# Kernel tuning notes

Hardware: AMD Instinct MI355X
Metric: run time of the kernel (lower is better)

## Reference

```python
import jax, jax.numpy as jnp
import numpy as np
from jax import lax

KS = 3      # generated depthwise kernel size
F = 9       # utils.FILTERS (channels)
P = 24      # utils.PSZ (patch size); conv stride 8 -> KS = P/8


def _extract_patches(x, p):
    # TF extract_patches with sizes=strides=p, VALID: (B,H,W,C) -> (B,nh,nw,p*p*C)
    B, H, W, C = x.shape
    nh, nw = H // p, W // p
    return (x.reshape(B, nh, p, nw, p, C)
             .transpose(0, 1, 3, 2, 4, 5)
             .reshape(B, nh, nw, p * p * C))


def setup_inputs() -> dict:
    key = jax.random.key(0)
    ks = jax.random.split(key, 6)
    B, H, Wd = 16, 384, 384
    return {
        "guidance": jax.random.normal(ks[0], (B, H, Wd, F), jnp.float32),
        "depth": jax.random.normal(ks[1], (B, H, Wd, F), jnp.float32),
        "conv_w": jax.random.normal(ks[2], (KS, KS, F, 9), jnp.float32) * 0.05,
        "conv_b": jax.random.normal(ks[3], (9,), jnp.float32) * 0.05,
        "dense_w": jax.random.normal(ks[4], (F, F * F), jnp.float32) * 0.05,
        "dense_b": jax.random.normal(ks[5], (F * F,), jnp.float32) * 0.05,
    }


def _forward(guidance, depth, conv_w, conv_b, dense_w, dense_b):
    B, H, W, _ = guidance.shape
    NP = (H // P) * (W // P)
    NB = NP * B
    # raw TF reshape (B,nh,nw,P*P*F) -> (NP,B,P,P,F), reproduced faithfully
    gp = _extract_patches(guidance, P).reshape(NP, B, P, P, F)
    dp = _extract_patches(depth, P).reshape(NP, B, P, P, F)

    # --- KGL: per-patch kernel generation (vectorized over NP*B) ---
    gflat = gp.reshape(NB, P, P, F)
    c = lax.conv_general_dilated(gflat, conv_w, (8, 8), 'SAME',
                                 dimension_numbers=('NHWC', 'HWIO', 'NHWC')) + conv_b
    W_G1 = c.reshape(NP, B, KS, KS, F, 1)
    n1 = jnp.sqrt(jnp.sum(W_G1 * W_G1, axis=(2, 3), keepdims=True))
    W_G1 = W_G1 / jnp.maximum(n1, 1.0)          # tf.clip_by_norm(.., 1, axes=[1,2])

    gap = gp.mean(axis=(2, 3))                   # (NP,B,F)
    d = gap @ dense_w + dense_b                  # (NP,B,F*F)
    W_G2 = d.reshape(NP, B, 1, 1, F, F)
    n2 = jnp.sqrt(jnp.sum(W_G2 * W_G2, axis=(2, 3, 4), keepdims=True))
    W_G2 = W_G2 / jnp.maximum(n2, 1.0)           # clip_by_norm axes=[1,2,3]

    # --- per-sample dynamic depthwise conv (vmap over NP*B) ---
    dw_rhs = W_G1.reshape(NB, KS, KS, F, 1).transpose(0, 1, 2, 4, 3)  # HWIO, groups=F
    dflat = dp.reshape(NB, P, P, F)

    def dwconv(img, f):
        return lax.conv_general_dilated(img[None], f, (1, 1), 'SAME',
                                        dimension_numbers=('NHWC', 'HWIO', 'NHWC'),
                                        feature_group_count=F)[0]

    dc = jax.vmap(dwconv)(dflat, dw_rhs)         # (NB,P,P,F)

    # --- per-sample dynamic 1x1 cross-channel conv == matmul ---
    cc = jnp.einsum('npqi,nio->npqo', dc, W_G2.reshape(NB, F, F))
    # raw TF reshape (NP,B,P,P,F) -> (B,H,W,F), reproduced faithfully
    return cc.reshape(B, H, W, F)


def reference(guidance, depth, conv_w, conv_b, dense_w, dense_b):
    return _forward(guidance, depth, conv_w, conv_b, dense_w, dense_b)
```

## Files before the change

kernel.cpp:

```cpp
#include <hip/hip_runtime.h>
#include <stdint.h>


__global__ __launch_bounds__(256) void kgl_kernel(
    const float* __restrict__ g,
    const float* __restrict__ cw,
    const float* __restrict__ cb,
    const float* __restrict__ dw,
    const float* __restrict__ db,
    float* __restrict__ ws)
{
    __shared__ __align__(16) float sg[5184];
    __shared__ float cwf[729];
    __shared__ float cbf[9];
    __shared__ float dwf[729];
    __shared__ float dbf[81];
    __shared__ float cols[216];
    __shared__ float gapm[9];
    __shared__ float cful[81];
    __shared__ float dld[81];

    const int m = blockIdx.x;
    const int t = threadIdx.x;
    const int b0 = m >> 8, pi = (m >> 4) & 15, pj = m & 15;
    const long rowbase = ((long)(b0 * 384 + pi * 24)) * 3456 + (long)pj * 216;

    for (int task = t; task < 1296; task += 256) {
        int r = task / 54, c = task - r * 54;
        const float4* p = reinterpret_cast<const float4*>(g + rowbase + (long)r * 3456);
        reinterpret_cast<float4*>(sg + r * 216)[c] = p[c];
    }
    for (int idx = t; idx < 729; idx += 256) cwf[idx] = cw[idx];
    for (int idx = t; idx < 729; idx += 256) dwf[idx] = dw[idx];
    if (t < 9) cbf[t] = cb[t];
    if (t >= 32 && t < 113) dbf[t - 32] = db[t - 32];
    if (t < 216 && (t % 12) >= 9) ws[(long)m * 216 + t] = 0.0f;
    __syncthreads();

    if (t < 216) {
        float s = 0.f;
        #pragma unroll
        for (int r = 0; r < 24; ++r) s += sg[r * 216 + t];
        cols[t] = s;
    }
    __syncthreads();

    if (t < 81) {
        int o = t % 9, uv = t / 9, v = uv % 3, u = uv / 3;
        float acc = cbf[o];
        #pragma unroll
        for (int du = 0; du < 3; ++du)
        #pragma unroll
        for (int dv = 0; dv < 3; ++dv) {
            const float* gp2 = &sg[(u * 8 + du) * 216 + (v * 8 + dv) * 9];
            const float* wp  = &cwf[(du * 3 + dv) * 81 + o];
            #pragma unroll
            for (int ci = 0; ci < 9; ++ci) acc += gp2[ci] * wp[ci * 9];
        }
        cful[t] = acc;
    }
    if (t >= 216 && t < 225) {
        int f = t - 216; float s = 0.f;
        #pragma unroll
        for (int c = 0; c < 24; ++c) s += cols[c * 9 + f];
        gapm[f] = s * (1.0f / 576.0f);
    }
    __syncthreads();

    if (t < 81) {
        float acc = dbf[t];
        #pragma unroll
        for (int k = 0; k < 9; ++k) acc += gapm[k] * dwf[k * 81 + t];
        dld[t] = acc;
    }
    if (t >= 96 && t < 105) {
        int f = t - 96; float s = 0.f;
        #pragma unroll
        for (int k = 0; k < 9; ++k) { float c = cful[k * 9 + f]; s += c * c; }
        float scale = (s > 1.0f) ? (1.0f / sqrtf(s)) : 1.0f;
        float* wout = ws + (long)m * 216;
        #pragma unroll
        for (int k = 0; k < 9; ++k) wout[k * 12 + f] = cful[k * 9 + f] * scale;
    }
    __syncthreads();

    if (t < 9) {
        float s = 0.f;
        #pragma unroll
        for (int i = 0; i < 9; ++i) { float d = dld[i * 9 + t]; s += d * d; }
        float scale = (s > 1.0f) ? (1.0f / sqrtf(s)) : 1.0f;
        float* wout = ws + (long)m * 216 + 108;
        #pragma unroll
        for (int i = 0; i < 9; ++i) wout[t * 12 + i] = dld[i * 9 + t] * scale;
    }
}

__global__ __launch_bounds__(576, 7) void apply_kernel(
    const float* __restrict__ dep,
    const float* __restrict__ ws,
    float* __restrict__ out)
{
    __shared__ __align__(16) float sd[8112];
    __shared__ float sw[216];

    const int m = blockIdx.x;
    const int t = threadIdx.x;
    const int b0 = m >> 8, pi = (m >> 4) & 15, pj = m & 15;
    const long rowbase = ((long)(b0 * 384 + pi * 24)) * 3456 + (long)pj * 216;

    if (t < 100) {
        int r, c;
        if (t < 26)      { r = 0;       c = t;      }
        else if (t < 52) { r = 25;      c = t - 26; }
        else if (t < 76) { r = t - 51;  c = 0;      }
        else             { r = t - 75;  c = 25;     }
        float4 z = make_float4(0.f, 0.f, 0.f, 0.f);
        float4* p = reinterpret_cast<float4*>(&sd[(r * 26 + c) * 12]);
        p[0] = z; p[1] = z; p[2] = z;
    }
    if (t >= 128 && t < 344) sw[t - 128] = ws[(long)m * 216 + (t - 128)];
    for (int task = t; task < 1296; task += 576) {
        int r = task / 54, c4 = task - r * 54;
        const float4* p = reinterpret_cast<const float4*>(dep + rowbase + (long)r * 3456);
        float4 v = p[c4];
        float vv[4] = { v.x, v.y, v.z, v.w };
        int e0 = c4 * 4;
        #pragma unroll
        for (int s = 0; s < 4; ++s) {
            int e = e0 + s;
            int col = e / 9, f = e - col * 9;
            sd[((r + 1) * 26 + (col + 1)) * 12 + f] = vv[s];
        }
    }
    __syncthreads();

    {
        const int row = t / 24;
        const int col = t - row * 24;
        float dc[9];
        #pragma unroll
        for (int i = 0; i < 9; ++i) dc[i] = 0.f;

        #pragma unroll
        for (int du = 0; du < 3; ++du)
        #pragma unroll
        for (int dv = 0; dv < 3; ++dv) {
            const float* sp = &sd[((row + du) * 26 + (col + dv)) * 12];
            const float* wv = &sw[(du * 3 + dv) * 12];
            float4 A = *reinterpret_cast<const float4*>(sp);
            float4 B = *reinterpret_cast<const float4*>(sp + 4);
            float a8 = sp[8];
            dc[0] += A.x * wv[0]; dc[1] += A.y * wv[1]; dc[2] += A.z * wv[2];
            dc[3] += A.w * wv[3]; dc[4] += B.x * wv[4]; dc[5] += B.y * wv[5];
            dc[6] += B.z * wv[6]; dc[7] += B.w * wv[7]; dc[8] += a8  * wv[8];
        }

        float* op = out + (long)m * 5184 + t * 9;
        #pragma unroll
        for (int o = 0; o < 9; ++o) {
            const float* wv = &sw[108 + o * 12];
            float a = 0.f;
            #pragma unroll
            for (int i = 0; i < 9; ++i) a += dc[i] * wv[i];
            op[o] = a;
        }
    }
}

extern "C" void kernel_launch(void* const* d_in, const int* in_sizes, int n_in,
                              void* d_out, int out_size, void* d_ws, size_t ws_size,
                              hipStream_t stream) {
    const float* g  = (const float*)d_in[0];
    const float* dp = (const float*)d_in[1];
    const float* cw = (const float*)d_in[2];
    const float* cb = (const float*)d_in[3];
    const float* dw = (const float*)d_in[4];
    const float* db = (const float*)d_in[5];
    float* ws = (float*)d_ws;
    float* out = (float*)d_out;

    kgl_kernel<<<dim3(4096), dim3(256), 0, stream>>>(g, cw, cb, dw, db, ws);
    apply_kernel<<<dim3(4096), dim3(576), 0, stream>>>(dp, ws, out);
}
```

Measured before the change: 253.0 us.

## Fuse kernel generation and dynamic conv into one kernel with async LDS loads

Merges the kernel-generation and apply kernels into a single 576-thread kernel, so the generated per-patch weights stay in shared memory and never round-trip through the global workspace. Guidance and depth tiles are loaded straight into LDS with global_load_lds. The padded depth tile is replaced by a dense one with bounds checks in the depthwise loop. Stage merging cuts one barrier, and the dense matmul normalisation now runs on only 9 threads. The costs are higher LDS use per block (occupancy bound lowered to 6) and branchy border handling.

```diff
diff --git a/kernel.cpp b/kernel.cpp
--- a/kernel.cpp
+++ b/kernel.cpp
@@ -2,39 +2,48 @@
 #include <stdint.h>
 
 
-__global__ __launch_bounds__(256) void kgl_kernel(
+__device__ __forceinline__ void gload16(const float* gsrc, float* ldst) {
+    __builtin_amdgcn_global_load_lds(
+        (__attribute__((address_space(1))) void*)gsrc,
+        (__attribute__((address_space(3))) void*)ldst, 16, 0, 0);
+}
+
+__global__ __launch_bounds__(576, 6) void fused_kernel(
     const float* __restrict__ g,
+    const float* __restrict__ dep,
     const float* __restrict__ cw,
     const float* __restrict__ cb,
     const float* __restrict__ dw,
     const float* __restrict__ db,
-    float* __restrict__ ws)
+    float* __restrict__ out)
 {
     __shared__ __align__(16) float sg[5184];
-    __shared__ float cwf[729];
+    __shared__ __align__(16) float sd[5184];
+    __shared__ __align__(16) float cwf[729];
+    __shared__ __align__(16) float dwf[729];
     __shared__ float cbf[9];
-    __shared__ float dwf[729];
     __shared__ float dbf[81];
     __shared__ float cols[216];
     __shared__ float gapm[9];
     __shared__ float cful[81];
-    __shared__ float dld[81];
+    __shared__ __align__(16) float sw[216];
 
     const int m = blockIdx.x;
     const int t = threadIdx.x;
     const int b0 = m >> 8, pi = (m >> 4) & 15, pj = m & 15;
     const long rowbase = ((long)(b0 * 384 + pi * 24)) * 3456 + (long)pj * 216;
 
-    for (int task = t; task < 1296; task += 256) {
-        int r = task / 54, c = task - r * 54;
-        const float4* p = reinterpret_cast<const float4*>(g + rowbase + (long)r * 3456);
-        reinterpret_cast<float4*>(sg + r * 216)[c] = p[c];
+    for (int task = t; task < 1296; task += 576) {
+        int r = task / 54, c4 = task - r * 54;
+        gload16(g + rowbase + (long)r * 3456 + c4 * 4, sg + task * 4);
     }
-    for (int idx = t; idx < 729; idx += 256) cwf[idx] = cw[idx];
-    for (int idx = t; idx < 729; idx += 256) dwf[idx] = dw[idx];
+    for (int task = t; task < 1296; task += 576) {
+        int r = task / 54, c4 = task - r * 54;
+        gload16(dep + rowbase + (long)r * 3456 + c4 * 4, sd + task * 4);
+    }
+    for (int idx = t; idx < 729; idx += 576) { cwf[idx] = cw[idx]; dwf[idx] = dw[idx]; }
     if (t < 9) cbf[t] = cb[t];
-    if (t >= 32 && t < 113) dbf[t - 32] = db[t - 32];
-    if (t < 216 && (t % 12) >= 9) ws[(long)m * 216 + t] = 0.0f;
+    if (t >= 64 && t < 145) dbf[t - 64] = db[t - 64];
     __syncthreads();
 
     if (t < 216) {
@@ -42,11 +51,9 @@
         #pragma unroll
         for (int r = 0; r < 24; ++r) s += sg[r * 216 + t];
         cols[t] = s;
-    }
-    __syncthreads();
-
-    if (t < 81) {
-        int o = t % 9, uv = t / 9, v = uv % 3, u = uv / 3;
+    } else if (t >= 256 && t < 337) {
+        const int q = t - 256;
+        const int o = q % 9, uv = q / 9, v = uv % 3, u = uv / 3;
         float acc = cbf[o];
         #pragma unroll
         for (int du = 0; du < 3; ++du)
@@ -57,80 +64,42 @@
             #pragma unroll
             for (int ci = 0; ci < 9; ++ci) acc += gp2[ci] * wp[ci * 9];
         }
-        cful[t] = acc;
-    }
-    if (t >= 216 && t < 225) {
-        int f = t - 216; float s = 0.f;
-        #pragma unroll
-        for (int c = 0; c < 24; ++c) s += cols[c * 9 + f];
-        gapm[f] = s * (1.0f / 576.0f);
-    }
-    __syncthreads();
-
-    if (t < 81) {
-        float acc = dbf[t];
-        #pragma unroll
-        for (int k = 0; k < 9; ++k) acc += gapm[k] * dwf[k * 81 + t];
-        dld[t] = acc;
-    }
-    if (t >= 96 && t < 105) {
-        int f = t - 96; float s = 0.f;
-        #pragma unroll
-        for (int k = 0; k < 9; ++k) { float c = cful[k * 9 + f]; s += c * c; }
-        float scale = (s > 1.0f) ? (1.0f / sqrtf(s)) : 1.0f;
-        float* wout = ws + (long)m * 216;
-        #pragma unroll
-        for (int k = 0; k < 9; ++k) wout[k * 12 + f] = cful[k * 9 + f] * scale;
+        cful[q] = acc;
     }
     __syncthreads();
 
     if (t < 9) {
         float s = 0.f;
         #pragma unroll
-        for (int i = 0; i < 9; ++i) { float d = dld[i * 9 + t]; s += d * d; }
-        float scale = (s > 1.0f) ? (1.0f / sqrtf(s)) : 1.0f;
-        float* wout = ws + (long)m * 216 + 108;
+        for (int c = 0; c < 24; ++c) s += cols[c * 9 + t];
+        gapm[t] = s * (1.0f / 576.0f);
+    } else if (t >= 64 && t < 73) {
+        const int f = t - 64;
+        float s = 0.f;
         #pragma unroll
-        for (int i = 0; i < 9; ++i) wout[t * 12 + i] = dld[i * 9 + t] * scale;
+        for (int k = 0; k < 9; ++k) { float c = cful[k * 9 + f]; s += c * c; }
+        const float scale = (s > 1.0f) ? (1.0f / sqrtf(s)) : 1.0f;
+        #pragma unroll
+        for (int k = 0; k < 9; ++k) sw[k * 12 + f] = cful[k * 9 + f] * scale;
     }
-}
+    __syncthreads();
 
-__global__ __launch_bounds__(576, 7) void apply_kernel(
-    const float* __restrict__ dep,
-    const float* __restrict__ ws,
-    float* __restrict__ out)
-{
-    __shared__ __align__(16) float sd[8112];
-    __shared__ float sw[216];
-
-    const int m = blockIdx.x;
-    const int t = threadIdx.x;
-    const int b0 = m >> 8, pi = (m >> 4) & 15, pj = m & 15;
-    const long rowbase = ((long)(b0 * 384 + pi * 24)) * 3456 + (long)pj * 216;
-
-    if (t < 100) {
-        int r, c;
-        if (t < 26)      { r = 0;       c = t;      }
-        else if (t < 52) { r = 25;      c = t - 26; }
-        else if (t < 76) { r = t - 51;  c = 0;      }
-        else             { r = t - 75;  c = 25;     }
-        float4 z = make_float4(0.f, 0.f, 0.f, 0.f);
-        float4* p = reinterpret_cast<float4*>(&sd[(r * 26 + c) * 12]);
-        p[0] = z; p[1] = z; p[2] = z;
-    }
-    if (t >= 128 && t < 344) sw[t - 128] = ws[(long)m * 216 + (t - 128)];
-    for (int task = t; task < 1296; task += 576) {
-        int r = task / 54, c4 = task - r * 54;
-        const float4* p = reinterpret_cast<const float4*>(dep + rowbase + (long)r * 3456);
-        float4 v = p[c4];
-        float vv[4] = { v.x, v.y, v.z, v.w };
-        int e0 = c4 * 4;
+    if (t < 9) {
+        float gv[9];
         #pragma unroll
-        for (int s = 0; s < 4; ++s) {
-            int e = e0 + s;
-            int col = e / 9, f = e - col * 9;
-            sd[((r + 1) * 26 + (col + 1)) * 12 + f] = vv[s];
+        for (int k = 0; k < 9; ++k) gv[k] = gapm[k];
+        float d[9];
+        float s = 0.f;
+        #pragma unroll
+        for (int i = 0; i < 9; ++i) {
+            float a = dbf[i * 9 + t];
+            #pragma unroll
+            for (int k = 0; k < 9; ++k) a += gv[k] * dwf[k * 81 + i * 9 + t];
+            d[i] = a; s += a * a;
         }
+        const float scale = (s > 1.0f) ? (1.0f / sqrtf(s)) : 1.0f;
+        #pragma unroll
+        for (int i = 0; i < 9; ++i) sw[108 + t * 12 + i] = d[i] * scale;
     }
     __syncthreads();
 
@@ -142,17 +111,18 @@
         for (int i = 0; i < 9; ++i) dc[i] = 0.f;
 
         #pragma unroll
-        for (int du = 0; du < 3; ++du)
-        #pragma unroll
-        for (int dv = 0; dv < 3; ++dv) {
-            const float* sp = &sd[((row + du) * 26 + (col + dv)) * 12];
-            const float* wv = &sw[(du * 3 + dv) * 12];
-            float4 A = *reinterpret_cast<const float4*>(sp);
-            float4 B = *reinterpret_cast<const float4*>(sp + 4);
-            float a8 = sp[8];
-            dc[0] += A.x * wv[0]; dc[1] += A.y * wv[1]; dc[2] += A.z * wv[2];
-            dc[3] += A.w * wv[3]; dc[4] += B.x * wv[4]; dc[5] += B.y * wv[5];
-            dc[6] += B.z * wv[6]; dc[7] += B.w * wv[7]; dc[8] += a8  * wv[8];
+        for (int du = 0; du < 3; ++du) {
+            const int r = row + du - 1;
+            if (r < 0 || r > 23) continue;
+            #pragma unroll
+            for (int dv = 0; dv < 3; ++dv) {
+                const int c = col + dv - 1;
+                if (c < 0 || c > 23) continue;
+                const float* sp = &sd[r * 216 + c * 9];
+                const float* wv = &sw[(du * 3 + dv) * 12];
+                #pragma unroll
+                for (int i = 0; i < 9; ++i) dc[i] += sp[i] * wv[i];
+            }
         }
 
         float* op = out + (long)m * 5184 + t * 9;
@@ -176,9 +146,8 @@
     const float* cb = (const float*)d_in[3];
     const float* dw = (const float*)d_in[4];
     const float* db = (const float*)d_in[5];
-    float* ws = (float*)d_ws;
     float* out = (float*)d_out;
+    (void)d_ws; (void)ws_size;
 
-    kgl_kernel<<<dim3(4096), dim3(256), 0, stream>>>(g, cw, cb, dw, db, ws);
-    apply_kernel<<<dim3(4096), dim3(576), 0, stream>>>(dp, ws, out);
+    fused_kernel<<<dim3(4096), dim3(576), 0, stream>>>(g, dp, cw, cb, dw, db, out);
 }
```

Result: faster. 237.9 us (-6.0%).
